# Optimization experiments

Hardware: AMD Instinct MI355X
Metric: run time of the kernel (lower is better)

Reference implementation:

```python
import jax, jax.numpy as jnp
import numpy as np

B, S, D, K = 4, 4096, 1024, 64

def setup_inputs() -> dict:
    key = jax.random.key(0)
    kx, kq, kk, kv, ko = jax.random.split(key, 5)
    scale = 1.0 / np.sqrt(D)
    return {
        "x": jax.random.normal(kx, (B, S, D), dtype=jnp.float32),
        "Wq": jax.random.uniform(kq, (K, D), dtype=jnp.float32, minval=-scale, maxval=scale),
        "Wk": jax.random.uniform(kk, (K, D), dtype=jnp.float32, minval=-scale, maxval=scale),
        "Wv": jax.random.uniform(kv, (K, D), dtype=jnp.float32, minval=-scale, maxval=scale),
        "Wo": jax.random.uniform(ko, (D, K), dtype=jnp.float32, minval=-1.0/np.sqrt(K), maxval=1.0/np.sqrt(K)),
    }

def reference(x, Wq, Wk, Wv, Wo):
    # projections: torch Linear(dim, key_dim, bias=False) -> x @ W.T
    Q = jax.nn.elu(x @ Wq.T) + 1.0          # [B,S,K]
    Kf = jax.nn.elu(x @ Wk.T) + 1.0         # [B,S,K]
    V = x @ Wv.T                             # [B,S,K]
    # causal running KV state via cumsum of outer products: [B,S,K,K]
    KV_sum = jnp.cumsum(Kf[..., :, None] * V[..., None, :], axis=1)
    K_sum = jnp.cumsum(Kf, axis=1)           # [B,S,K]
    num = jnp.einsum('bsk,bskm->bsm', Q, KV_sum)   # [B,S,K]
    den = jnp.einsum('bsk,bsk->bs', Q, K_sum)[..., None]
    out = num / (den + 1e-6)
    return out @ Wo.T                         # [B,S,D]
```

## Files before the change

### kernel.cpp

```cpp
#include <hip/hip_runtime.h>

#define BB 4
#define SS 4096
#define DDIM 1024
#define KDIM 64
#define NCHUNK 64
#define TCHUNK 256
#define MROWS 16384

typedef short short8v __attribute__((ext_vector_type(8)));
typedef float f32x4 __attribute__((ext_vector_type(4)));
#define MFMA16 __builtin_amdgcn_mfma_f32_16x16x32_bf16

#define GLDS16(gp, lp) __builtin_amdgcn_global_load_lds( \
    (const __attribute__((address_space(1))) unsigned int*)(gp), \
    (__attribute__((address_space(3))) unsigned int*)(lp), 16, 0, 0)

__device__ __forceinline__ ushort f2bf(float f) {
    uint u = __float_as_uint(f);
    u += 0x7FFFu + ((u >> 16) & 1u);
    return (ushort)(u >> 16);
}

__device__ __forceinline__ uint cvtpk(float lo, float hi) {
    uint r;
    asm("v_cvt_pk_bf16_f32 %0, %1, %2" : "=v"(r) : "v"(lo), "v"(hi));
    return r;
}

__global__ __launch_bounds__(256) void k_wconv(
    const float* __restrict__ Wq, const float* __restrict__ Wk,
    const float* __restrict__ Wv, const float* __restrict__ Wo,
    ushort* __restrict__ Whf, ushort* __restrict__ Wof)
{
    const int b = blockIdx.x, t = threadIdx.x;
    const int ks = t >> 7;
    const int l = (t >> 1) & 63;
    const int half = t & 1;
    if (b < 192) {
        const int s = b / 12, cf = b % 12;
        const int grow = cf * 16 + (l & 15);
        const int gcol = s * 64 + ks * 32 + ((l >> 4) & 3) * 8 + half * 4;
        const float* src = (grow < 64) ? (Wq + (size_t)grow * DDIM)
                         : (grow < 128) ? (Wk + (size_t)(grow - 64) * DDIM)
                                        : (Wv + (size_t)(grow - 128) * DDIM);
        float4 v = *(const float4*)&src[gcol];
        ushort* dst = &Whf[(size_t)(((s * 12 + cf) * 2 + ks) * 64 + l) * 8 + half * 4];
        dst[0] = f2bf(v.x); dst[1] = f2bf(v.y); dst[2] = f2bf(v.z); dst[3] = f2bf(v.w);
    } else {
        const int cf = b - 192;
        const int d = cf * 16 + (l & 15);
        const int kc = ks * 32 + ((l >> 4) & 3) * 8 + half * 4;
        float4 v = *(const float4*)&Wo[(size_t)d * KDIM + kc];
        ushort* dst = &Wof[(size_t)((cf * 2 + ks) * 64 + l) * 8 + half * 4];
        dst[0] = f2bf(v.x); dst[1] = f2bf(v.y); dst[2] = f2bf(v.z); dst[3] = f2bf(v.w);
    }
}

#define EBP 216
__global__ __launch_bounds__(512, 2) void k_proj(
    const float* __restrict__ x, const ushort* __restrict__ Whf,
    ushort* __restrict__ Qf, ushort* __restrict__ Kff,
    ushort* __restrict__ KfT, ushort* __restrict__ VT)
{
    __shared__ ushort lds[2][14336];
    const int t = threadIdx.x;
    const int w = t >> 6, l = t & 63;
    const int rw = w >> 2, cw = w & 3;
    const int mb = blockIdx.x;
    const int row0 = mb * 32;
    const int lq = l >> 4;

    const int xr = t >> 4;
    const int xc = (t & 15) * 4;
    const float* xbase = &x[(size_t)(row0 + xr) * DDIM + xc];
    const int xslot = (((xr >> 4) * 2 + (xc >> 5)) * 64
                       + ((xr & 15) | (((xc >> 3) & 3) << 4))) * 8 + ((xc >> 2) & 1) * 4;

    auto ldX = [&](int s) -> float4 { return *(const float4*)(xbase + s * 64); };
    auto stX = [&](float4 v, int buf) {
        uint2 pk;
        pk.x = cvtpk(v.x, v.y);
        pk.y = cvtpk(v.z, v.w);
        *(uint2*)&lds[buf][xslot] = pk;
    };
    auto stageW = [&](int s, int buf) {
#pragma unroll
        for (int ii = 0; ii < 3; ++ii) {
            const int f = w * 3 + ii;
            const ushort* gp = &Whf[(size_t)(s * 24 + f) * 512 + l * 8];
            GLDS16(gp, &lds[buf][2048 + f * 512]);
        }
    };

    f32x4 acc[3];
#pragma unroll
    for (int c = 0; c < 3; ++c) acc[c] = (f32x4){0.f, 0.f, 0.f, 0.f};

    auto compute = [&](int buf) {
#pragma unroll
        for (int ks = 0; ks < 2; ++ks) {
            short8v a = *(const short8v*)&lds[buf][((rw * 2 + ks) * 64 + l) * 8];
#pragma unroll
            for (int c = 0; c < 3; ++c) {
                short8v b = *(const short8v*)&lds[buf][2048 + ((cw * 3 + c) * 2 + ks) * 512 + l * 8];
                acc[c] = MFMA16(a, b, acc[c], 0, 0, 0);
            }
        }
    };

    float4 xe = ldX(0);
    float4 xo = ldX(1);
    stageW(0, 0);
    stX(xe, 0);
    __syncthreads();
#pragma unroll
    for (int s2 = 0; s2 < 16; s2 += 2) {
        if (s2 + 2 < 16) xe = ldX(s2 + 2);
        if (s2 + 1 < 16) stageW(s2 + 1, 1);
        compute(0);
        if (s2 + 1 < 16) stX(xo, 1);
        __syncthreads();
        if (s2 + 3 < 16) xo = ldX(s2 + 3);
        if (s2 + 2 < 16) stageW(s2 + 2, 0);
        if (s2 + 1 < 16) compute(1);
        if (s2 + 2 < 16) stX(xe, 0);
        __syncthreads();
    }

    ushort* eb = &lds[0][0];
#pragma unroll
    for (int c = 0; c < 3; ++c) {
        const int col = (cw * 3 + c) * 16 + (l & 15);
#pragma unroll
        for (int q = 0; q < 4; ++q) {
            const int row = rw * 16 + lq * 4 + q;
            float v = acc[c][q];
            if (col < 128) v = (v > 0.f) ? v + 1.f : __expf(v);
            eb[row * EBP + col] = f2bf(v);
        }
    }
    __syncthreads();

    {
        const int which = w >> 2, rf = (w >> 1) & 1, ks = w & 1;
        const int r = rf * 16 + (l & 15);
        const int c0 = ks * 32 + ((l >> 4) & 3) * 8 + (which ? 64 : 0);
        short8v v8 = *(const short8v*)&eb[r * EBP + c0];
        const size_t fo = ((size_t)(mb * 4 + rf * 2 + ks)) * 512 + l * 8;
        if (which == 0) *(short8v*)&Qf[fo] = v8;
        else            *(short8v*)&Kff[fo] = v8;
    }
    {
        const int which = w >> 2, f = w & 3;
        const int col = (which ? 128 : 64) + f * 16 + (l & 15);
        const int jb = ((l >> 4) & 3) * 8;
        short8v tv;
#pragma unroll
        for (int e = 0; e < 8; ++e) tv[e] = (short)eb[(jb + e) * EBP + col];
        const size_t fo = ((size_t)((mb >> 1) * 8 + f * 2 + (mb & 1))) * 512 + l * 8;
        if (which == 0) *(short8v*)&KfT[fo] = tv;
        else            *(short8v*)&VT[fo]  = tv;
    }
}

__global__ __launch_bounds__(64) void k_chunksum(
    const ushort* __restrict__ KfT, const ushort* __restrict__ VT,
    float* __restrict__ KVc, float* __restrict__ Ksc)
{
    const int g = blockIdx.x, l = threadIdx.x;
    short8v ka[4][2], vb[4][2];
#pragma unroll
    for (int f = 0; f < 4; ++f)
#pragma unroll
        for (int js = 0; js < 2; ++js) {
            const size_t fo = ((size_t)(g * 8 + f * 2 + js)) * 512 + l * 8;
            ka[f][js] = *(const short8v*)&KfT[fo];
            vb[f][js] = *(const short8v*)&VT[fo];
        }
    short8v onesf;
#pragma unroll
    for (int e = 0; e < 8; ++e) onesf[e] = ((l & 15) == 0) ? (short)0x3F80 : (short)0;

    f32x4 acc[4][5];
#pragma unroll
    for (int kf = 0; kf < 4; ++kf)
#pragma unroll
        for (int mf = 0; mf < 5; ++mf) acc[kf][mf] = (f32x4){0.f, 0.f, 0.f, 0.f};
#pragma unroll
    for (int js = 0; js < 2; ++js)
#pragma unroll
        for (int kf = 0; kf < 4; ++kf) {
#pragma unroll
            for (int mf = 0; mf < 4; ++mf)
                acc[kf][mf] = MFMA16(ka[kf][js], vb[mf][js], acc[kf][mf], 0, 0, 0);
            acc[kf][4] = MFMA16(ka[kf][js], onesf, acc[kf][4], 0, 0, 0);
        }
    const int lq = l >> 4;
#pragma unroll
    for (int kf = 0; kf < 4; ++kf) {
#pragma unroll
        for (int q = 0; q < 4; ++q) {
            const int k = kf * 16 + lq * 4 + q;
#pragma unroll
            for (int mf = 0; mf < 4; ++mf)
                KVc[(size_t)g * 4096 + k * 64 + mf * 16 + (l & 15)] = acc[kf][mf][q];
            if ((l & 15) == 0) Ksc[(size_t)g * KDIM + k] = acc[kf][4][q];
        }
    }
}

__global__ void k_scan(const float* __restrict__ KVc, const float* __restrict__ Ksc,
                       float* __restrict__ Sst, float* __restrict__ Kss)
{
    const int b = blockIdx.x / 65;
    const int r = blockIdx.x % 65;
    const int t = threadIdx.x;
    if (r < 64) {
        const int e = r * 64 + t;
        float v[64];
#pragma unroll
        for (int i = 0; i < 64; ++i)
            v[i] = KVc[((size_t)(b * NCHUNK + i)) * 4096 + e];
        float acc = 0.f;
#pragma unroll
        for (int i = 0; i < 64; ++i) {
            Sst[((size_t)(b * NCHUNK + i)) * 4096 + e] = acc;
            acc += v[i];
        }
    } else {
        float v[64];
#pragma unroll
        for (int i = 0; i < 64; ++i)
            v[i] = Ksc[((size_t)(b * NCHUNK + i)) * KDIM + t];
        float acc = 0.f;
#pragma unroll
        for (int i = 0; i < 64; ++i) {
            Kss[((size_t)(b * NCHUNK + i)) * KDIM + t] = acc;
            acc += v[i];
        }
    }
}

__global__ __launch_bounds__(256) void k_intra(
    const ushort* __restrict__ Qf, const ushort* __restrict__ Kff,
    const ushort* __restrict__ VT, const float* __restrict__ Sst,
    const float* __restrict__ Kss, const ushort* __restrict__ Wof,
    float* __restrict__ out)
{
    __shared__ ushort pb[32 * 64];
    __shared__ ushort sT[80 * 64];
    __shared__ float ob[4][16 * 68 + 4];
    const int bx = blockIdx.x, t = threadIdx.x;
    const int g = bx >> 1, rh = bx & 1;
    const int w = t >> 6, l = t & 63;
    const int lq = l >> 4;

    {
        const int k = t >> 2, m0 = (t & 3) * 16;
        const float4* sp = (const float4*)&Sst[(size_t)g * 4096 + k * 64 + m0];
        float4 f0 = sp[0], f1 = sp[1], f2v = sp[2], f3 = sp[3];
        float fv[16] = {f0.x, f0.y, f0.z, f0.w, f1.x, f1.y, f1.z, f1.w,
                        f2v.x, f2v.y, f2v.z, f2v.w, f3.x, f3.y, f3.z, f3.w};
#pragma unroll
        for (int i = 0; i < 16; ++i) {
            const int m = m0 + i;
            sT[m * 64 + (k ^ ((m & 7) << 3))] = f2bf(fv[i]);
        }
        if (t < 64) sT[64 * 64 + t] = f2bf(Kss[(size_t)g * KDIM + t]);
        for (int idx = t; idx < 960; idx += 256) sT[65 * 64 + idx] = 0;
    }

    const int rf = w & 1;
    short8v qa[2];
#pragma unroll
    for (int ks = 0; ks < 2; ++ks)
        qa[ks] = *(const short8v*)&Qf[((size_t)((g * 2 + rh) * 4 + rf * 2 + ks)) * 512 + l * 8];
    {
        const int cfh = w >> 1;
        f32x4 accs[2];
#pragma unroll
        for (int ci = 0; ci < 2; ++ci) accs[ci] = (f32x4){0.f, 0.f, 0.f, 0.f};
#pragma unroll
        for (int ci = 0; ci < 2; ++ci) {
            const int cf = cfh * 2 + ci;
#pragma unroll
            for (int ks = 0; ks < 2; ++ks) {
                short8v kb = *(const short8v*)&Kff[((size_t)((g * 2 + (cf >> 1)) * 4 + (cf & 1) * 2 + ks)) * 512 + l * 8];
                accs[ci] = MFMA16(qa[ks], kb, accs[ci], 0, 0, 0);
            }
        }
#pragma unroll
        for (int ci = 0; ci < 2; ++ci)
#pragma unroll
            for (int q = 0; q < 4; ++q) {
                const int row = rf * 16 + lq * 4 + q;
                const int col = (cfh * 2 + ci) * 16 + (l & 15);
                const float sv = (col <= rh * 32 + row) ? accs[ci][q] : 0.f;
                pb[row * 64 + (col ^ ((row & 7) << 3))] = f2bf(sv);
            }
    }
    __syncthreads();

    const int mg = w >> 1;
    f32x4 an0 = (f32x4){0.f,0.f,0.f,0.f}, an1 = (f32x4){0.f,0.f,0.f,0.f};
    f32x4 ad = (f32x4){0.f,0.f,0.f,0.f};
    short8v onesf;
#pragma unroll
    for (int e = 0; e < 8; ++e) onesf[e] = ((l & 15) == 0) ? (short)0x3F80 : (short)0;
#pragma unroll
    for (int js = 0; js < 2; ++js) {
        const int prow = rf * 16 + (l & 15);
        const int pbase = js * 32 + ((l >> 4) & 3) * 8;
        short8v pa = *(const short8v*)&pb[prow * 64 + (pbase ^ ((prow & 7) << 3))];
        short8v v0 = *(const short8v*)&VT[((size_t)(g * 8 + (mg * 2 + 0) * 2 + js)) * 512 + l * 8];
        short8v v1 = *(const short8v*)&VT[((size_t)(g * 8 + (mg * 2 + 1) * 2 + js)) * 512 + l * 8];
        an0 = MFMA16(pa, v0, an0, 0, 0, 0);
        an1 = MFMA16(pa, v1, an1, 0, 0, 0);
        ad  = MFMA16(pa, onesf, ad, 0, 0, 0);
    }
#pragma unroll
    for (int ks = 0; ks < 2; ++ks) {
        const int base = ks * 32 + ((l >> 4) & 3) * 8;
        const int r0 = (mg * 2 + 0) * 16 + (l & 15);
        const int r1 = (mg * 2 + 1) * 16 + (l & 15);
        const int r4 = 64 + (l & 15);
        short8v s0 = *(const short8v*)&sT[r0 * 64 + (base ^ ((r0 & 7) << 3))];
        short8v s1 = *(const short8v*)&sT[r1 * 64 + (base ^ ((r1 & 7) << 3))];
        short8v s4 = *(const short8v*)&sT[r4 * 64 + (base ^ ((r4 & 7) << 3))];
        an0 = MFMA16(qa[ks], s0, an0, 0, 0, 0);
        an1 = MFMA16(qa[ks], s1, an1, 0, 0, 0);
        ad  = MFMA16(qa[ks], s4, ad, 0, 0, 0);
    }
#pragma unroll
    for (int q = 0; q < 4; ++q) {
        const float den = __shfl(ad[q], (l & 48));
        const float rinv = 1.f / (den + 1e-6f);
        const int row = rf * 16 + lq * 4 + q;
        const int c0 = (mg * 2 + 0) * 16 + (l & 15);
        const int c1 = (mg * 2 + 1) * 16 + (l & 15);
        pb[row * 64 + (c0 ^ ((row & 7) << 3))] = f2bf(an0[q] * rinv);
        pb[row * 64 + (c1 ^ ((row & 7) << 3))] = f2bf(an1[q] * rinv);
    }
    __syncthreads();

    short8v oa[2][2];
#pragma unroll
    for (int rfi = 0; rfi < 2; ++rfi)
#pragma unroll
        for (int ks = 0; ks < 2; ++ks) {
            const int row = rfi * 16 + (l & 15);
            const int base = ks * 32 + ((l >> 4) & 3) * 8;
            oa[rfi][ks] = *(const short8v*)&pb[row * 64 + (base ^ ((row & 7) << 3))];
        }
    float* obw = ob[w];
#pragma unroll
    for (int rr = 0; rr < 4; ++rr) {
        f32x4 acco[2][4];
#pragma unroll
        for (int rfi = 0; rfi < 2; ++rfi)
#pragma unroll
            for (int ci = 0; ci < 4; ++ci) acco[rfi][ci] = (f32x4){0.f, 0.f, 0.f, 0.f};
#pragma unroll
        for (int ci = 0; ci < 4; ++ci) {
            const int cfg = w * 16 + rr * 4 + ci;
#pragma unroll
            for (int ks = 0; ks < 2; ++ks) {
                short8v wb = *(const short8v*)&Wof[((size_t)(cfg * 2 + ks)) * 512 + l * 8];
#pragma unroll
                for (int rfi = 0; rfi < 2; ++rfi)
                    acco[rfi][ci] = MFMA16(oa[rfi][ks], wb, acco[rfi][ci], 0, 0, 0);
            }
        }
#pragma unroll
        for (int rfi = 0; rfi < 2; ++rfi) {
#pragma unroll
            for (int ci = 0; ci < 4; ++ci)
#pragma unroll
                for (int q = 0; q < 4; ++q)
                    obw[(lq * 4 + q) * 68 + ci * 16 + (l & 15)] = acco[rfi][ci][q];
#pragma unroll
            for (int rg = 0; rg < 4; ++rg) {
                const int row = rg * 4 + lq;
                float4 vv = *(const float4*)&obw[row * 68 + (l & 15) * 4];
                *(float4*)&out[((size_t)(g * 64 + rh * 32 + rfi * 16 + row)) * DDIM
                               + w * 256 + rr * 64 + (l & 15) * 4] = vv;
            }
        }
    }
}

extern "C" void kernel_launch(void* const* d_in, const int* in_sizes, int n_in,
                              void* d_out, int out_size, void* d_ws, size_t ws_size,
                              hipStream_t stream)
{
    const float* x  = (const float*)d_in[0];
    const float* Wq = (const float*)d_in[1];
    const float* Wk = (const float*)d_in[2];
    const float* Wv = (const float*)d_in[3];
    const float* Wo = (const float*)d_in[4];
    float* out = (float*)d_out;

    float* ws   = (float*)d_ws;
    float* KVc  = ws;
    float* Sst  = KVc + (size_t)TCHUNK * 4096;
    float* Ksc  = Sst + (size_t)TCHUNK * 4096;
    float* Kss  = Ksc + (size_t)TCHUNK * KDIM;
    ushort* Whf = (ushort*)(Kss + (size_t)TCHUNK * KDIM);
    ushort* Wof = Whf + (size_t)192 * DDIM;
    ushort* Qf  = Wof + (size_t)64 * 1024;
    ushort* Kff = Qf  + (size_t)512 * 4 * 512;
    ushort* KfT = Kff + (size_t)512 * 4 * 512;
    ushort* VT  = KfT + (size_t)256 * 8 * 512;

    k_wconv<<<dim3(256), dim3(256), 0, stream>>>(Wq, Wk, Wv, Wo, Whf, Wof);
    k_proj<<<dim3(MROWS / 32), dim3(512), 0, stream>>>(x, Whf, Qf, Kff, KfT, VT);
    k_chunksum<<<dim3(TCHUNK), dim3(64), 0, stream>>>(KfT, VT, KVc, Ksc);
    k_scan<<<dim3(BB * 65), dim3(64), 0, stream>>>(KVc, Ksc, Sst, Kss);
    k_intra<<<dim3(TCHUNK * 2), dim3(256), 0, stream>>>(Qf, Kff, VT, Sst, Kss, Wof, out);
}
```

Measured before the change: 52.09 us.

## Halve projection LDS footprint by loading second-k weight fragments straight to registers

Result: no change. 52.13 us (+0.1%).

```diff
diff --git a/kernel.cpp b/kernel.cpp
--- a/kernel.cpp
+++ b/kernel.cpp
@@ -58,12 +58,12 @@
 }
 
 #define EBP 216
-__global__ __launch_bounds__(512, 2) void k_proj(
+__global__ __launch_bounds__(512, 4) void k_proj(
     const float* __restrict__ x, const ushort* __restrict__ Whf,
     ushort* __restrict__ Qf, ushort* __restrict__ Kff,
     ushort* __restrict__ KfT, ushort* __restrict__ VT)
 {
-    __shared__ ushort lds[2][14336];
+    __shared__ ushort lds[2][8192];
     const int t = threadIdx.x;
     const int w = t >> 6, l = t & 63;
     const int rw = w >> 2, cw = w & 3;
@@ -85,28 +85,39 @@
         *(uint2*)&lds[buf][xslot] = pk;
     };
     auto stageW = [&](int s, int buf) {
-#pragma unroll
-        for (int ii = 0; ii < 3; ++ii) {
-            const int f = w * 3 + ii;
-            const ushort* gp = &Whf[(size_t)(s * 24 + f) * 512 + l * 8];
-            GLDS16(gp, &lds[buf][2048 + f * 512]);
+        if (w < 8) {
+            const ushort* gp = &Whf[(size_t)(s * 24 + w * 2) * 512 + l * 8];
+            GLDS16(gp, &lds[buf][2048 + w * 512]);
+        }
+        if (w < 4) {
+            const int cf = 8 + w;
+            const ushort* gp = &Whf[(size_t)(s * 24 + cf * 2) * 512 + l * 8];
+            GLDS16(gp, &lds[buf][2048 + cf * 512]);
         }
     };
+    auto loadBwr = [&](int s, short8v (&bwr)[3]) {
+#pragma unroll
+        for (int c = 0; c < 3; ++c)
+            bwr[c] = *(const short8v*)&Whf[(size_t)(s * 24 + (cw * 3 + c) * 2 + 1) * 512 + l * 8];
+    };
 
     f32x4 acc[3];
 #pragma unroll
     for (int c = 0; c < 3; ++c) acc[c] = (f32x4){0.f, 0.f, 0.f, 0.f};
 
-    auto compute = [&](int buf) {
-#pragma unroll
-        for (int ks = 0; ks < 2; ++ks) {
-            short8v a = *(const short8v*)&lds[buf][((rw * 2 + ks) * 64 + l) * 8];
-#pragma unroll
-            for (int c = 0; c < 3; ++c) {
-                short8v b = *(const short8v*)&lds[buf][2048 + ((cw * 3 + c) * 2 + ks) * 512 + l * 8];
-                acc[c] = MFMA16(a, b, acc[c], 0, 0, 0);
-            }
-        }
+    auto computeHalf0 = [&](int buf) {
+        short8v a0 = *(const short8v*)&lds[buf][((rw * 2 + 0) * 64 + l) * 8];
+#pragma unroll
+        for (int c = 0; c < 3; ++c) {
+            short8v b = *(const short8v*)&lds[buf][2048 + (cw * 3 + c) * 512 + l * 8];
+            acc[c] = MFMA16(a0, b, acc[c], 0, 0, 0);
+        }
+    };
+    auto computeHalf1 = [&](int buf, short8v (&bwr)[3]) {
+        short8v a1 = *(const short8v*)&lds[buf][((rw * 2 + 1) * 64 + l) * 8];
+#pragma unroll
+        for (int c = 0; c < 3; ++c)
+            acc[c] = MFMA16(a1, bwr[c], acc[c], 0, 0, 0);
     };
 
     float4 xe = ldX(0);
@@ -116,15 +127,25 @@
     __syncthreads();
 #pragma unroll
     for (int s2 = 0; s2 < 16; s2 += 2) {
-        if (s2 + 2 < 16) xe = ldX(s2 + 2);
-        if (s2 + 1 < 16) stageW(s2 + 1, 1);
-        compute(0);
-        if (s2 + 1 < 16) stX(xo, 1);
+        {
+            short8v bwr[3];
+            loadBwr(s2, bwr);
+            stageW(s2 + 1, 1);
+            if (s2 + 2 < 16) xe = ldX(s2 + 2);
+            computeHalf0(0);
+            stX(xo, 1);
+            computeHalf1(0, bwr);
+        }
         __syncthreads();
-        if (s2 + 3 < 16) xo = ldX(s2 + 3);
-        if (s2 + 2 < 16) stageW(s2 + 2, 0);
-        if (s2 + 1 < 16) compute(1);
-        if (s2 + 2 < 16) stX(xe, 0);
+        {
+            short8v bwr[3];
+            loadBwr(s2 + 1, bwr);
+            if (s2 + 2 < 16) stageW(s2 + 2, 0);
+            if (s2 + 3 < 16) xo = ldX(s2 + 3);
+            computeHalf0(1);
+            if (s2 + 2 < 16) stX(xe, 0);
+            computeHalf1(1, bwr);
+        }
         __syncthreads();
     }
 
```
